# Optimization experiments

Measured on AMD Instinct MI355X. Metric: run time of the kernel, lower is better.

The kernel has to match this reference:

```python
import jax, jax.numpy as jnp
import numpy as np


def setup_inputs() -> dict:
    key = jax.random.key(0)
    ks = jax.random.split(key, 4)
    B, T, M, E, F = 4, 2048, 1024, 8, 4096
    hidden_states = jax.random.normal(ks[0], (B, T, M), dtype=jnp.float32)
    wg = jax.random.normal(ks[1], (M, E), dtype=jnp.float32) * (1.0 / np.sqrt(M))
    w1 = jax.random.normal(ks[2], (E, M, F), dtype=jnp.float32) * (1.0 / np.sqrt(M))
    b1 = jnp.zeros((E, F), dtype=jnp.float32)
    w2 = jax.random.normal(ks[3], (E, F, M), dtype=jnp.float32) * (1.0 / np.sqrt(F))
    b2 = jnp.zeros((E, M), dtype=jnp.float32)
    return {"hidden_states": hidden_states, "wg": wg, "w1": w1, "b1": b1, "w2": w2, "b2": b2}


def reference(hidden_states, wg, w1, b1, w2, b2):
    B, T, M = hidden_states.shape
    E = wg.shape[1]
    S = B * T
    MIN_CAPACITY = 4
    C = max((S + E - 1) // E, MIN_CAPACITY)  # capacity_factor = 1 (static)

    x = hidden_states.reshape(S, M)  # [S, M]

    # --- top-1 gating (deepspeed TopKGate, noisy=None, use_rts=False) ---
    logits = x @ wg                                  # [S, E]
    gates = jax.nn.softmax(logits, axis=-1)          # [S, E]
    idx = jnp.argmax(gates, axis=-1)                 # [S]
    mask1 = jax.nn.one_hot(idx, E, dtype=gates.dtype)  # [S, E]
    # aux loss (computed before capacity drop)
    l_aux = jnp.sum(gates.mean(0) * mask1.mean(0)) * E
    # position of each token within its expert's queue
    locations1 = jnp.cumsum(mask1, axis=0) - 1.0     # [S, E]
    mask1 = mask1 * (locations1 < C)                 # drop overflow tokens
    gates1_s = jnp.sum(gates * mask1, axis=1)        # [S]
    loc_s = jnp.sum(locations1 * mask1, axis=1).astype(jnp.int32)  # [S]
    loc_sc = jax.nn.one_hot(loc_s, C, dtype=gates.dtype)           # [S, C]

    combine_weights = jnp.einsum('se,sc->sec', gates1_s[:, None] * mask1, loc_sc)  # [S,E,C]
    dispatch_mask = (combine_weights > 0).astype(x.dtype)

    # --- dispatch ---
    dispatched = jnp.einsum('sec,sm->ecm', dispatch_mask, x)  # [E, C, M]

    # --- expert FFN (grouped GEMM) ---
    h = jax.nn.gelu(jnp.einsum('ecm,emf->ecf', dispatched, w1) + b1[:, None, :])
    expert_out = jnp.einsum('ecf,efm->ecm', h, w2) + b2[:, None, :]  # [E, C, M]

    # --- combine ---
    out = jnp.einsum('sec,ecm->sm', combine_weights, expert_out)  # [S, M]
    return out.reshape(B, T, M)
```

## Files before the change

kernel.cpp:

```cpp
#include <hip/hip_runtime.h>
#include <hip/hip_bf16.h>
#include <math.h>

#define S_TOK 8192
#define M_DIM 1024
#define E_NUM 8
#define F_DIM 4096
#define CAP   1024

typedef short short8 __attribute__((ext_vector_type(8)));
typedef float f32x4 __attribute__((ext_vector_type(4)));
typedef unsigned short ushortx4 __attribute__((ext_vector_type(4)));

__device__ inline unsigned short f2bf(float f) {
    union { float f; unsigned int u; } v; v.f = f;
    unsigned int r = v.u + 0x7fffu + ((v.u >> 16) & 1u);
    return (unsigned short)(r >> 16);
}

__device__ inline float gelu_fast(float x) {
    float y = 0.7978845608028654f * (x + 0.044715f * x * x * x);
    if (y > 40.f) return x;
    float e = exp2f(2.8853900817779268f * y);
    return x * e / (e + 1.0f);
}

__device__ inline void gl_lds16(const void* g, void* l) {
    __builtin_amdgcn_global_load_lds(
        (const __attribute__((address_space(1))) unsigned int*)g,
        (__attribute__((address_space(3))) unsigned int*)l, 16, 0, 0);
}

__global__ __launch_bounds__(256) void gating_kernel(
    const float* __restrict__ x, const float* __restrict__ wg,
    int* __restrict__ idx, float* __restrict__ gate)
{
    int wid = threadIdx.x >> 6;
    int lane = threadIdx.x & 63;
    int s = blockIdx.x * 4 + wid;
    const float* xs = x + (size_t)s * M_DIM;

    double acc[E_NUM];
#pragma unroll
    for (int e = 0; e < E_NUM; e++) acc[e] = 0.0;

    for (int i = lane; i < M_DIM; i += 64) {
        float xv = xs[i];
        float4 wa = *(const float4*)(wg + (size_t)i * E_NUM);
        float4 wb = *(const float4*)(wg + (size_t)i * E_NUM + 4);
        acc[0] += (double)xv * (double)wa.x;
        acc[1] += (double)xv * (double)wa.y;
        acc[2] += (double)xv * (double)wa.z;
        acc[3] += (double)xv * (double)wa.w;
        acc[4] += (double)xv * (double)wb.x;
        acc[5] += (double)xv * (double)wb.y;
        acc[6] += (double)xv * (double)wb.z;
        acc[7] += (double)xv * (double)wb.w;
    }
#pragma unroll
    for (int e = 0; e < E_NUM; e++) {
        double v = acc[e];
        for (int o = 32; o > 0; o >>= 1) v += __shfl_down(v, o, 64);
        acc[e] = v;
    }
    if (lane == 0) {
        double mx = acc[0]; int am = 0;
#pragma unroll
        for (int e = 1; e < E_NUM; e++) {
            if (acc[e] > mx) { mx = acc[e]; am = e; }
        }
        double se = 0.0;
#pragma unroll
        for (int e = 0; e < E_NUM; e++) se += exp(acc[e] - mx);
        idx[s] = am;
        gate[s] = (float)(1.0 / se);
    }
}

__global__ __launch_bounds__(1024) void scan_build(
    const int* __restrict__ idx, int* __restrict__ srcmap)
{
    __shared__ unsigned int sc[2][4][1024];
    int t = threadIdx.x;

    for (int i = t; i < E_NUM * CAP; i += 1024) srcmap[i] = -1;

    int eid[8];
    unsigned int cnt[E_NUM];
#pragma unroll
    for (int e = 0; e < E_NUM; e++) cnt[e] = 0;
#pragma unroll
    for (int i = 0; i < 8; i++) {
        int e = idx[t * 8 + i];
        eid[i] = e;
        cnt[e]++;
    }
    unsigned int pk[4];
#pragma unroll
    for (int i = 0; i < 4; i++) pk[i] = cnt[2 * i] | (cnt[2 * i + 1] << 16);
#pragma unroll
    for (int i = 0; i < 4; i++) sc[0][i][t] = pk[i];

    int buf = 0;
    for (int ofs = 1; ofs < 1024; ofs <<= 1) {
        __syncthreads();
        unsigned int v[4];
#pragma unroll
        for (int i = 0; i < 4; i++) {
            v[i] = sc[buf][i][t] + ((t >= ofs) ? sc[buf][i][t - ofs] : 0u);
            sc[buf ^ 1][i][t] = v[i];
        }
        buf ^= 1;
    }
    __syncthreads();
    unsigned int pos[E_NUM];
#pragma unroll
    for (int e = 0; e < E_NUM; e++) {
        unsigned int incl = (sc[buf][e >> 1][t] >> ((e & 1) * 16)) & 0xffffu;
        pos[e] = incl - cnt[e];
    }
#pragma unroll
    for (int i = 0; i < 8; i++) {
        int e = eid[i];
        unsigned int p = pos[e]++;
        if (p < CAP) srcmap[e * CAP + p] = t * 8 + i;
    }
}

__global__ __launch_bounds__(256) void dispatch_kernel(
    const float* __restrict__ x, const int* __restrict__ srcmap,
    unsigned short* __restrict__ A1)
{
    int slot = blockIdx.x;
    int s = srcmap[slot];
    int t = threadIdx.x;
    ushortx4 o;
    if (s >= 0) {
        float4 v = ((const float4*)(x + (size_t)s * M_DIM))[t];
        o[0] = f2bf(v.x); o[1] = f2bf(v.y); o[2] = f2bf(v.z); o[3] = f2bf(v.w);
    } else {
        o[0] = 0; o[1] = 0; o[2] = 0; o[3] = 0;
    }
    ((ushortx4*)(A1 + (size_t)slot * M_DIM))[t] = o;
}

__global__ __launch_bounds__(256) void transpose_cvt(
    const float* __restrict__ in, unsigned short* __restrict__ out, int R, int Cc)
{
    __shared__ float tile[32][33];
    int e = blockIdx.z;
    int br = blockIdx.y * 32, bc = blockIdx.x * 32;
    const float* ine = in + (size_t)e * R * Cc;
    unsigned short* oute = out + (size_t)e * R * Cc;
    int tx = threadIdx.x, ty = threadIdx.y;
#pragma unroll
    for (int i = 0; i < 32; i += 8)
        tile[ty + i][tx] = ine[(size_t)(br + ty + i) * Cc + (bc + tx)];
    __syncthreads();
#pragma unroll
    for (int i = 0; i < 32; i += 8)
        oute[(size_t)(bc + ty + i) * R + (br + tx)] = f2bf(tile[tx][ty + i]);
}

template <int MODE>
__global__ __launch_bounds__(1024, 1) void gemm256sq(
    const unsigned short* __restrict__ A, const unsigned short* __restrict__ B,
    const float* __restrict__ bias, unsigned short* __restrict__ OutH,
    float* __restrict__ OutP)
{
    constexpr int K    = (MODE == 0) ? 1024 : 4096;
    constexpr int NB   = (MODE == 0) ? 4096 : 1024;
    constexpr int KLEN = (MODE == 0) ? 1024 : 2048;
    constexpr int NT   = KLEN / 32;
    constexpr int NWG  = (MODE == 0) ? 512 : 256;
    constexpr int SLOT = 16384;

    __shared__ __align__(16) unsigned short LDS[3 * SLOT];

    int bid = blockIdx.x;
    int swz = (bid & 7) * (NWG / 8) + (bid >> 3);
    int e, tm, tn, ks;
    if (MODE == 0) {
        e = swz >> 6; int r = swz & 63; tn = r >> 2; tm = r & 3; ks = 0;
    } else {
        e = swz >> 5; int r = swz & 31; ks = r >> 4; int rr = r & 15;
        tm = rr >> 2; tn = rr & 3;
    }
    int kOff = (MODE == 0) ? 0 : ks * 2048;

    const unsigned short* Ae = A + ((size_t)e * CAP + (size_t)tm * 256) * K + kOff;
    const unsigned short* Be = B + ((size_t)e * NB + (size_t)tn * 256) * K + kOff;

    int tid = threadIdx.x, w = tid >> 6, lane = tid & 63;
    int wm = w >> 2, wn = w & 3;
    int fr = lane & 15, kq = lane >> 4;

    int lr2 = lane >> 2, sl4 = lane & 3;
    int lc = sl4 ^ (lr2 & 3);
    const unsigned short* gA = Ae + (size_t)(w * 16 + lr2) * K + lc * 8;
    const unsigned short* gB = Be + (size_t)(w * 16 + lr2) * K + lc * 8;
    int dA = (w * 16) * 32;
    int dB = 8192 + (w * 16) * 32;

#define STAGE(sl, t_) do { int ko_ = (t_) * 32;                      \
    gl_lds16(gA + ko_, &LDS[(sl) * SLOT + dA]);                      \
    gl_lds16(gB + ko_, &LDS[(sl) * SLOT + dB]);                      \
} while (0)

    int swc = ((kq ^ (fr & 3)) << 3);
    int aoff = (wm * 64 + fr) * 32 + swc;
    int boff = 8192 + (wn * 64 + fr) * 32 + swc;

    f32x4 acc[4][4];
#pragma unroll
    for (int i = 0; i < 4; i++)
#pragma unroll
        for (int j = 0; j < 4; j++) acc[i][j] = (f32x4){0.f, 0.f, 0.f, 0.f};

    STAGE(0, 0);
    STAGE(1, 1);
    asm volatile("s_waitcnt vmcnt(2)" ::: "memory");
    __builtin_amdgcn_s_barrier();

    int cur = 0, stg = 2;
#pragma unroll 1
    for (int t = 0; t < NT; ++t) {
        if (t + 2 < NT) STAGE(stg, t + 2);

        int sb = cur * SLOT;
        short8 a[4], b[4];
#pragma unroll
        for (int mi = 0; mi < 4; mi++)
            a[mi] = *(const short8*)&LDS[sb + aoff + mi * 512];
#pragma unroll
        for (int ni = 0; ni < 4; ni++)
            b[ni] = *(const short8*)&LDS[sb + boff + ni * 512];
        __builtin_amdgcn_s_setprio(1);
#pragma unroll
        for (int mi = 0; mi < 4; mi++)
#pragma unroll
            for (int ni = 0; ni < 4; ni++)
                acc[mi][ni] = __builtin_amdgcn_mfma_f32_16x16x32_bf16(
                    a[mi], b[ni], acc[mi][ni], 0, 0, 0);
        __builtin_amdgcn_s_setprio(0);

        if (t + 2 < NT)      asm volatile("s_waitcnt vmcnt(2)" ::: "memory");
        else if (t + 1 < NT) asm volatile("s_waitcnt vmcnt(0)" ::: "memory");
        __builtin_amdgcn_s_barrier();
        cur = (cur + 1 == 3) ? 0 : cur + 1;
        stg = (stg + 1 == 3) ? 0 : stg + 1;
    }
#undef STAGE

    if (MODE == 0) {
        unsigned short* R = (unsigned short*)LDS;
        float bv[4];
#pragma unroll
        for (int ni = 0; ni < 4; ni++)
            bv[ni] = bias[e * NB + tn * 256 + wn * 64 + ni * 16 + fr];
#pragma unroll 1
        for (int h = 0; h < 2; ++h) {
            __syncthreads();
            if ((wm >> 1) == h) {
#pragma unroll
                for (int mi = 0; mi < 4; mi++) {
#pragma unroll
                    for (int j = 0; j < 4; j++) {
                        int row = (wm & 1) * 64 + mi * 16 + kq * 4 + j;
#pragma unroll
                        for (int ni = 0; ni < 4; ni++) {
                            int col = wn * 64 + ni * 16 + fr;
                            R[row * 256 + (((col >> 3) ^ (row & 7)) << 3) + (col & 7)] =
                                f2bf(gelu_fast(acc[mi][ni][j] + bv[ni]));
                        }
                    }
                }
            }
            __syncthreads();
            int row = tid >> 3, seg = tid & 7;
            size_t gb = ((size_t)(e * CAP + tm * 256 + h * 128 + row)) * NB
                        + tn * 256 + seg * 32;
#pragma unroll
            for (int i = 0; i < 4; i++) {
                int chunk = seg * 4 + i;
                *(short8*)&OutH[gb + i * 8] =
                    *(const short8*)&R[row * 256 + ((chunk ^ (row & 7)) << 3)];
            }
        }
    } else {
        float* OP = OutP + (size_t)ks * S_TOK * M_DIM;
#pragma unroll
        for (int mi = 0; mi < 4; mi++) {
#pragma unroll
            for (int j = 0; j < 4; j++) {
                int r = tm * 256 + wm * 64 + mi * 16 + kq * 4 + j;
                size_t rowbase = ((size_t)(e * CAP + r)) * NB + tn * 256 + wn * 64;
#pragma unroll
                for (int ni = 0; ni < 4; ni++)
                    OP[rowbase + ni * 16 + fr] = acc[mi][ni][j];
            }
        }
    }
}

__global__ __launch_bounds__(256) void combine_kernel(
    const float* __restrict__ P, const int* __restrict__ srcmap,
    const float* __restrict__ gate, const float* __restrict__ b2,
    float* __restrict__ out)
{
    int r = blockIdx.x;
    int s = srcmap[r];
    if (s < 0) return;
    int e = r >> 10;
    float g = gate[s];
    int t = threadIdx.x;
    float4 p0 = ((const float4*)P)[r * 256 + t];
    float4 p1 = ((const float4*)(P + (size_t)S_TOK * M_DIM))[r * 256 + t];
    float4 bb = ((const float4*)b2)[e * 256 + t];
    float4 o;
    o.x = g * (p0.x + p1.x + bb.x);
    o.y = g * (p0.y + p1.y + bb.y);
    o.z = g * (p0.z + p1.z + bb.z);
    o.w = g * (p0.w + p1.w + bb.w);
    ((float4*)out)[s * 256 + t] = o;
}

extern "C" void kernel_launch(void* const* d_in, const int* in_sizes, int n_in,
                              void* d_out, int out_size, void* d_ws, size_t ws_size,
                              hipStream_t stream) {
    const float* x  = (const float*)d_in[0];
    const float* wg = (const float*)d_in[1];
    const float* w1 = (const float*)d_in[2];
    const float* b1 = (const float*)d_in[3];
    const float* w2 = (const float*)d_in[4];
    const float* b2 = (const float*)d_in[5];
    float* out = (float*)d_out;

    char* ws = (char*)d_ws;
    unsigned short* A1  = (unsigned short*)(ws);
    unsigned short* W1T = (unsigned short*)(ws + (size_t)(16u << 20));
    float*          P   = (float*)(ws + (size_t)(16u << 20));
    unsigned short* W2T = (unsigned short*)(ws + (size_t)(80u << 20));
    unsigned short* H   = (unsigned short*)(ws + (size_t)(144u << 20));
    int*   idx  = (int*)(ws + (size_t)(208u << 20));
    float* gate = (float*)(ws + (size_t)(208u << 20) + 32768);
    int*   srcm = (int*)(ws + (size_t)(208u << 20) + 65536);

    hipMemsetAsync(d_out, 0, (size_t)S_TOK * M_DIM * sizeof(float), stream);

    gating_kernel<<<S_TOK / 4, 256, 0, stream>>>(x, wg, idx, gate);
    scan_build<<<1, 1024, 0, stream>>>(idx, srcm);
    dispatch_kernel<<<E_NUM * CAP, 256, 0, stream>>>(x, srcm, A1);
    transpose_cvt<<<dim3(F_DIM / 32, M_DIM / 32, E_NUM), dim3(32, 8), 0, stream>>>(
        w1, W1T, M_DIM, F_DIM);
    transpose_cvt<<<dim3(M_DIM / 32, F_DIM / 32, E_NUM), dim3(32, 8), 0, stream>>>(
        w2, W2T, F_DIM, M_DIM);

    gemm256sq<0><<<512, 1024, 0, stream>>>(A1, W1T, b1, H, nullptr);

    gemm256sq<1><<<256, 1024, 0, stream>>>(H, W2T, nullptr, nullptr, P);

    combine_kernel<<<E_NUM * CAP, 256, 0, stream>>>(P, srcm, gate, b2, out);
}
```

Before: 381.1 us.

## Halve GEMM workgroup to 512 threads with 128x64 warp tiles, two blocks per CU

The 256x256 expert GEMM tile is now computed by 8 waves instead of 16. Each wave owns a 128x64 sub-tile with 32 accumulators, and each thread issues four global-to-LDS loads per stage. Launch bounds allow two workgroups per CU, so one block's barriers and LDS waits can overlap with another's MFMA work, and each LDS B-fragment read feeds more MFMAs. The LDS swizzle pattern and the tm/tn order for the second GEMM also change. The cost is much higher register pressure, which risks spills or failing to actually fit two blocks per CU alongside 96KB of LDS each.

Measured after the change: 402.9 us. 1.06x slower.

```diff
diff --git a/kernel.cpp b/kernel.cpp
--- a/kernel.cpp
+++ b/kernel.cpp
@@ -163,7 +163,7 @@
 }
 
 template <int MODE>
-__global__ __launch_bounds__(1024, 1) void gemm256sq(
+__global__ __launch_bounds__(512, 2) void gemm256(
     const unsigned short* __restrict__ A, const unsigned short* __restrict__ B,
     const float* __restrict__ bias, unsigned short* __restrict__ OutH,
     float* __restrict__ OutP)
@@ -184,9 +184,9 @@
         e = swz >> 6; int r = swz & 63; tn = r >> 2; tm = r & 3; ks = 0;
     } else {
         e = swz >> 5; int r = swz & 31; ks = r >> 4; int rr = r & 15;
-        tm = rr >> 2; tn = rr & 3;
-    }
-    int kOff = (MODE == 0) ? 0 : ks * 2048;
+        tn = rr >> 2; tm = rr & 3;
+    }
+    size_t kOff = (MODE == 0) ? 0 : (size_t)ks * 2048;
 
     const unsigned short* Ae = A + ((size_t)e * CAP + (size_t)tm * 256) * K + kOff;
     const unsigned short* Be = B + ((size_t)e * NB + (size_t)tn * 256) * K + kOff;
@@ -195,31 +195,36 @@
     int wm = w >> 2, wn = w & 3;
     int fr = lane & 15, kq = lane >> 4;
 
-    int lr2 = lane >> 2, sl4 = lane & 3;
-    int lc = sl4 ^ (lr2 & 3);
-    const unsigned short* gA = Ae + (size_t)(w * 16 + lr2) * K + lc * 8;
-    const unsigned short* gB = Be + (size_t)(w * 16 + lr2) * K + lc * 8;
-    int dA = (w * 16) * 32;
-    int dB = 8192 + (w * 16) * 32;
-
-#define STAGE(sl, t_) do { int ko_ = (t_) * 32;                      \
-    gl_lds16(gA + ko_, &LDS[(sl) * SLOT + dA]);                      \
-    gl_lds16(gB + ko_, &LDS[(sl) * SLOT + dB]);                      \
+    int lr = lane >> 2;
+    int srow = w * 16 + lr;
+    int q = (((srow >> 1) ^ lane) & 3);
+    const unsigned short* gA = Ae + (size_t)srow * K + q * 8;
+    const unsigned short* gB = Be + (size_t)srow * K + q * 8;
+    int dA0 = (w * 16) * 32;
+    int dA1 = (128 + w * 16) * 32;
+    int dB0 = 8192 + (w * 16) * 32;
+    int dB1 = 8192 + (128 + w * 16) * 32;
+
+#define STAGE(sl, t_) do { size_t ko_ = (size_t)(t_) * 32;                    \
+    gl_lds16(gA + ko_,                    &LDS[(sl) * SLOT + dA0]);           \
+    gl_lds16(gA + (size_t)128 * K + ko_,  &LDS[(sl) * SLOT + dA1]);           \
+    gl_lds16(gB + ko_,                    &LDS[(sl) * SLOT + dB0]);           \
+    gl_lds16(gB + (size_t)128 * K + ko_,  &LDS[(sl) * SLOT + dB1]);           \
 } while (0)
 
-    int swc = ((kq ^ (fr & 3)) << 3);
-    int aoff = (wm * 64 + fr) * 32 + swc;
+    int swc = (((fr >> 1) ^ kq) & 3) << 3;
+    int aoff = (wm * 128 + fr) * 32 + swc;
     int boff = 8192 + (wn * 64 + fr) * 32 + swc;
 
-    f32x4 acc[4][4];
-#pragma unroll
-    for (int i = 0; i < 4; i++)
+    f32x4 acc[8][4];
+#pragma unroll
+    for (int i = 0; i < 8; i++)
 #pragma unroll
         for (int j = 0; j < 4; j++) acc[i][j] = (f32x4){0.f, 0.f, 0.f, 0.f};
 
     STAGE(0, 0);
     STAGE(1, 1);
-    asm volatile("s_waitcnt vmcnt(2)" ::: "memory");
+    asm volatile("s_waitcnt vmcnt(4)" ::: "memory");
     __builtin_amdgcn_s_barrier();
 
     int cur = 0, stg = 2;
@@ -228,23 +233,23 @@
         if (t + 2 < NT) STAGE(stg, t + 2);
 
         int sb = cur * SLOT;
-        short8 a[4], b[4];
-#pragma unroll
-        for (int mi = 0; mi < 4; mi++)
+        short8 a[8], b[4];
+#pragma unroll
+        for (int mi = 0; mi < 8; mi++)
             a[mi] = *(const short8*)&LDS[sb + aoff + mi * 512];
 #pragma unroll
         for (int ni = 0; ni < 4; ni++)
             b[ni] = *(const short8*)&LDS[sb + boff + ni * 512];
         __builtin_amdgcn_s_setprio(1);
 #pragma unroll
-        for (int mi = 0; mi < 4; mi++)
+        for (int mi = 0; mi < 8; mi++)
 #pragma unroll
             for (int ni = 0; ni < 4; ni++)
                 acc[mi][ni] = __builtin_amdgcn_mfma_f32_16x16x32_bf16(
                     a[mi], b[ni], acc[mi][ni], 0, 0, 0);
         __builtin_amdgcn_s_setprio(0);
 
-        if (t + 2 < NT)      asm volatile("s_waitcnt vmcnt(2)" ::: "memory");
+        if (t + 2 < NT)      asm volatile("s_waitcnt vmcnt(4)" ::: "memory");
         else if (t + 1 < NT) asm volatile("s_waitcnt vmcnt(0)" ::: "memory");
         __builtin_amdgcn_s_barrier();
         cur = (cur + 1 == 3) ? 0 : cur + 1;
@@ -261,12 +266,12 @@
 #pragma unroll 1
         for (int h = 0; h < 2; ++h) {
             __syncthreads();
-            if ((wm >> 1) == h) {
-#pragma unroll
-                for (int mi = 0; mi < 4; mi++) {
+            if (wm == h) {
+#pragma unroll
+                for (int mi = 0; mi < 8; mi++) {
 #pragma unroll
                     for (int j = 0; j < 4; j++) {
-                        int row = (wm & 1) * 64 + mi * 16 + kq * 4 + j;
+                        int row = mi * 16 + (kq << 2) + j;
 #pragma unroll
                         for (int ni = 0; ni < 4; ni++) {
                             int col = wn * 64 + ni * 16 + fr;
@@ -277,12 +282,12 @@
                 }
             }
             __syncthreads();
-            int row = tid >> 3, seg = tid & 7;
+            int row = tid >> 2, seg = tid & 3;
             size_t gb = ((size_t)(e * CAP + tm * 256 + h * 128 + row)) * NB
-                        + tn * 256 + seg * 32;
-#pragma unroll
-            for (int i = 0; i < 4; i++) {
-                int chunk = seg * 4 + i;
+                        + tn * 256 + seg * 64;
+#pragma unroll
+            for (int i = 0; i < 8; i++) {
+                int chunk = seg * 8 + i;
                 *(short8*)&OutH[gb + i * 8] =
                     *(const short8*)&R[row * 256 + ((chunk ^ (row & 7)) << 3)];
             }
@@ -290,10 +295,10 @@
     } else {
         float* OP = OutP + (size_t)ks * S_TOK * M_DIM;
 #pragma unroll
-        for (int mi = 0; mi < 4; mi++) {
+        for (int mi = 0; mi < 8; mi++) {
 #pragma unroll
             for (int j = 0; j < 4; j++) {
-                int r = tm * 256 + wm * 64 + mi * 16 + kq * 4 + j;
+                int r = tm * 256 + wm * 128 + mi * 16 + (kq << 2) + j;
                 size_t rowbase = ((size_t)(e * CAP + r)) * NB + tn * 256 + wn * 64;
 #pragma unroll
                 for (int ni = 0; ni < 4; ni++)
@@ -356,9 +361,9 @@
     transpose_cvt<<<dim3(M_DIM / 32, F_DIM / 32, E_NUM), dim3(32, 8), 0, stream>>>(
         w2, W2T, F_DIM, M_DIM);
 
-    gemm256sq<0><<<512, 1024, 0, stream>>>(A1, W1T, b1, H, nullptr);
-
-    gemm256sq<1><<<256, 1024, 0, stream>>>(H, W2T, nullptr, nullptr, P);
+    gemm256<0><<<512, 512, 0, stream>>>(A1, W1T, b1, H, nullptr);
+
+    gemm256<1><<<256, 512, 0, stream>>>(H, W2T, nullptr, nullptr, P);
 
     combine_kernel<<<E_NUM * CAP, 256, 0, stream>>>(P, srcm, gate, b2, out);
 }
```
